# Kernel optimization log

Hardware: AMD Instinct MI355X
Metric: run time of the kernel (lower is better)

The kernel has to match this reference:

```python
import jax, jax.numpy as jnp
import numpy as np

DIM = 384
NUM_HEADS = 8
HEAD_DIM = DIM // NUM_HEADS
SCALE = HEAD_DIM ** -0.5
MLP_HIDDEN = int(DIM * 4.0)
EPS = 1e-6


def setup_inputs() -> dict:
    key = jax.random.key(0)
    ks = jax.random.split(key, 8)
    s = 0.02
    return {
        "x": jax.random.normal(ks[0], (2, DIM, 8, 16, 16), dtype=jnp.float32),
        "g1": jnp.ones((DIM,), jnp.float32),
        "b1": jnp.zeros((DIM,), jnp.float32),
        "Wqkv": jax.random.normal(ks[1], (DIM, 3 * DIM), jnp.float32) * s,  # no bias (qkv_bias=False)
        "Wo": jax.random.normal(ks[2], (DIM, DIM), jnp.float32) * s,
        "bo": jnp.zeros((DIM,), jnp.float32),
        "g2": jnp.ones((DIM,), jnp.float32),
        "b2": jnp.zeros((DIM,), jnp.float32),
        "W1": jax.random.normal(ks[3], (DIM, MLP_HIDDEN), jnp.float32) * s,
        "b1m": jnp.zeros((MLP_HIDDEN,), jnp.float32),
        "W2": jax.random.normal(ks[4], (MLP_HIDDEN, DIM), jnp.float32) * s,
        "b2m": jnp.zeros((DIM,), jnp.float32),
    }


def _layernorm(x, g, b):
    mu = jnp.mean(x, axis=-1, keepdims=True)
    var = jnp.mean(jnp.square(x - mu), axis=-1, keepdims=True)
    return (x - mu) * jax.lax.rsqrt(var + EPS) * g + b


def _attention(h, Wqkv, Wo, bo):
    B, N, C = h.shape
    qkv = h @ Wqkv  # [B, N, 3C]
    qkv = qkv.reshape(B, N, 3, NUM_HEADS, HEAD_DIM).transpose(2, 0, 3, 1, 4)
    q, k, v = qkv[0], qkv[1], qkv[2]  # each [B, H, N, d]
    att = jax.nn.softmax(jnp.einsum('bhxd,bhyd->bhxy', q, k) * SCALE, axis=-1)
    out = jnp.einsum('bhxy,bhyd->bhxd', att, v)  # [B, H, N, d]
    out = out.transpose(0, 2, 1, 3).reshape(B, N, C)
    return out @ Wo + bo


def reference(x, g1, b1, Wqkv, Wo, bo, g2, b2, W1, b1m, W2, b2m):
    B, C, D, H, W = x.shape
    h = x.transpose(0, 2, 3, 4, 1).reshape(B, D * H * W, C)  # b (d h w) c
    h = h + _attention(_layernorm(h, g1, b1), Wqkv, Wo, bo)
    m = _layernorm(h, g2, b2)
    m = jax.nn.gelu(m @ W1 + b1m, approximate=False) @ W2 + b2m
    h = h + m
    return h.reshape(B, D, H, W, C).transpose(0, 4, 1, 2, 3)
```

## Files before the change

kernel.cpp:

```cpp
#include <hip/hip_runtime.h>
#include <hip/hip_bf16.h>
#include <math.h>

#define DIM    384
#define NHEAD  8
#define HDIM   48
#define NTOK   2048
#define BATCH  2
#define TOKS   (BATCH * NTOK)
#define HIDDEN 1536

typedef __bf16 bf16x8 __attribute__((ext_vector_type(8)));
typedef float  f32x4  __attribute__((ext_vector_type(4)));
typedef unsigned short u16;

union bfu { __hip_bfloat16 h; u16 u; };

__device__ __forceinline__ void load_lds16(const void* g, void* l) {
    __builtin_amdgcn_global_load_lds(
        (const __attribute__((address_space(1))) void*)g,
        (__attribute__((address_space(3))) void*)l, 16, 0, 0);
}

__global__ __launch_bounds__(256) void wtrans_all(
    const float* __restrict__ Wqkv, const float* __restrict__ Wo,
    const float* __restrict__ W1,   const float* __restrict__ W2,
    __hip_bfloat16* __restrict__ WqkvT, __hip_bfloat16* __restrict__ WoT,
    __hip_bfloat16* __restrict__ W1T,   __hip_bfloat16* __restrict__ W2T) {
    __shared__ float t[32][33];
    int id = blockIdx.x;
    const float* src; __hip_bfloat16* dst; int R, C;
    if (id < 432)       { src = Wqkv; dst = WqkvT; R = 384;  C = 1152; }
    else if (id < 576)  { id -= 432;  src = Wo;    dst = WoT;  R = 384;  C = 384; }
    else if (id < 1152) { id -= 576;  src = W1;    dst = W1T;  R = 384;  C = 1536; }
    else                { id -= 1152; src = W2;    dst = W2T;  R = 1536; C = 384; }
    int tc = C / 32;
    int i0 = (id / tc) * 32, j0 = (id % tc) * 32;
    int tx = threadIdx.x & 31, ty = threadIdx.x >> 5;
#pragma unroll
    for (int k = 0; k < 32; k += 8)
        t[ty + k][tx] = src[(size_t)(i0 + ty + k) * C + j0 + tx];
    __syncthreads();
#pragma unroll
    for (int k = 0; k < 32; k += 8)
        dst[(size_t)(j0 + ty + k) * R + i0 + tx] = __float2bfloat16(t[tx][ty + k]);
}

__global__ __launch_bounds__(256) void tln(const float* __restrict__ x,
                                           const float* __restrict__ g,
                                           const float* __restrict__ bta,
                                           float* __restrict__ hOut,
                                           __hip_bfloat16* __restrict__ y) {
    __shared__ float t[384 * 33];
    int n0 = blockIdx.x * 32, b = blockIdx.y;
    const float* xb = x + (size_t)b * DIM * NTOK;
    int tid = threadIdx.x;
    for (int idx = tid; idx < 384 * 32; idx += 256) {
        int c = idx >> 5, n = idx & 31;
        t[c * 33 + n] = xb[(size_t)c * NTOK + n0 + n];
    }
    __syncthreads();
    int wid = tid >> 6, lane = tid & 63;
#pragma unroll
    for (int it = 0; it < 8; ++it) {
        int tl = it * 4 + wid;
        float v[6];
        float s = 0.f;
#pragma unroll
        for (int i = 0; i < 6; ++i) { v[i] = t[(lane + 64 * i) * 33 + tl]; s += v[i]; }
#pragma unroll
        for (int o = 32; o; o >>= 1) s += __shfl_xor(s, o, 64);
        float mu = s * (1.f / DIM);
        float s2 = 0.f;
#pragma unroll
        for (int i = 0; i < 6; ++i) { float d = v[i] - mu; s2 += d * d; }
#pragma unroll
        for (int o = 32; o; o >>= 1) s2 += __shfl_xor(s2, o, 64);
        float r = rsqrtf(s2 * (1.f / DIM) + 1e-6f);
        size_t tok = (size_t)b * NTOK + n0 + tl;
#pragma unroll
        for (int i = 0; i < 6; ++i) {
            int c = lane + 64 * i;
            hOut[tok * DIM + c] = v[i];
            y[tok * DIM + c] = __float2bfloat16((v[i] - mu) * r * g[c] + bta[c]);
        }
    }
}

__global__ __launch_bounds__(256) void vtile(const u16* __restrict__ qkv,
                                             unsigned int* __restrict__ vt32) {
    __shared__ u16 t[128 * 49];
    int k0 = blockIdx.x * 128;
    int bh = blockIdx.y;
    int b = bh >> 3, h = bh & 7;
    int tid = threadIdx.x;
    const u16* src = qkv + (size_t)(b * NTOK + k0) * 1152 + 768 + h * 48;
#pragma unroll
    for (int idx = tid; idx < 768; idx += 256) {
        int r = idx / 6, c = idx % 6;
        uint4 v = *(const uint4*)(src + (size_t)r * 1152 + c * 8);
        u16* dst = &t[r * 49 + c * 8];
        dst[0] = (u16)(v.x & 0xffff); dst[1] = (u16)(v.x >> 16);
        dst[2] = (u16)(v.y & 0xffff); dst[3] = (u16)(v.y >> 16);
        dst[4] = (u16)(v.z & 0xffff); dst[5] = (u16)(v.z >> 16);
        dst[6] = (u16)(v.w & 0xffff); dst[7] = (u16)(v.w >> 16);
    }
    __syncthreads();
    unsigned int* outb = vt32 + (((size_t)bh * 48) * 2048 + k0) / 2;
#pragma unroll
    for (int idx = tid; idx < 3072; idx += 256) {
        int d = idx >> 6, pp = idx & 63;
        int k1 = (pp & 3) * 32 + (pp >> 2);
        unsigned int lo = t[k1 * 49 + d];
        unsigned int hi = t[(k1 + 16) * 49 + d];
        outb[(size_t)d * 1024 + pp] = lo | (hi << 16);
    }
}

__global__ __launch_bounds__(256) void ln_kernel(const float* __restrict__ x,
                                                 const float* __restrict__ g,
                                                 const float* __restrict__ bta,
                                                 __hip_bfloat16* __restrict__ y) {
    int wid = threadIdx.x >> 6, lane = threadIdx.x & 63;
    int tok = blockIdx.x * 4 + wid;
    const float* xr = x + (size_t)tok * DIM;
    float v[6];
    float s = 0.f;
#pragma unroll
    for (int i = 0; i < 6; ++i) { v[i] = xr[lane + 64 * i]; s += v[i]; }
#pragma unroll
    for (int o = 32; o; o >>= 1) s += __shfl_xor(s, o, 64);
    float mu = s * (1.f / DIM);
    float s2 = 0.f;
#pragma unroll
    for (int i = 0; i < 6; ++i) { float d = v[i] - mu; s2 += d * d; }
#pragma unroll
    for (int o = 32; o; o >>= 1) s2 += __shfl_xor(s2, o, 64);
    float r = rsqrtf(s2 * (1.f / DIM) + 1e-6f);
    __hip_bfloat16* yr = y + (size_t)tok * DIM;
#pragma unroll
    for (int i = 0; i < 6; ++i) {
        int c = lane + 64 * i;
        yr[c] = __float2bfloat16((v[i] - mu) * r * g[c] + bta[c]);
    }
}

template<bool GELU, bool BF16OUT, bool TRANSOUT>
__global__ __launch_bounds__(256) void gemm_mfma(
    const __hip_bfloat16* __restrict__ A,
    const __hip_bfloat16* __restrict__ BT,
    const float* __restrict__ bias,
    const float* __restrict__ res,
    void* __restrict__ Cout,
    int M, int N, int K) {
    __shared__ __align__(16) u16 As[64 * 32];
    __shared__ __align__(16) u16 Bs[64 * 32];
    int bm = blockIdx.y * 64, bn = blockIdx.x * 64;
    int tid = threadIdx.x;
    int w = tid >> 6, l = tid & 63;
    int m0 = (w >> 1) * 32, n0 = (w & 1) * 32;
    int lm = l & 15, ksel = l >> 4;

    int row = tid >> 2, c16 = tid & 3;
    const __hip_bfloat16* ga = A  + (size_t)(bm + row) * K + c16 * 8;
    const __hip_bfloat16* gb = BT + (size_t)(bn + row) * K + c16 * 8;
    u16* la = &As[tid * 8];
    u16* lb = &Bs[tid * 8];

    f32x4 acc[2][2] = {};
    for (int k0 = 0; k0 < K; k0 += 32) {
        load_lds16(ga + k0, la);
        load_lds16(gb + k0, lb);
        __syncthreads();
        bf16x8 af0 = *(const bf16x8*)&As[(m0 +      lm) * 32 + ksel * 8];
        bf16x8 af1 = *(const bf16x8*)&As[(m0 + 16 + lm) * 32 + ksel * 8];
        bf16x8 bf0 = *(const bf16x8*)&Bs[(n0 +      lm) * 32 + ksel * 8];
        bf16x8 bf1 = *(const bf16x8*)&Bs[(n0 + 16 + lm) * 32 + ksel * 8];
        acc[0][0] = __builtin_amdgcn_mfma_f32_16x16x32_bf16(af0, bf0, acc[0][0], 0, 0, 0);
        acc[0][1] = __builtin_amdgcn_mfma_f32_16x16x32_bf16(af0, bf1, acc[0][1], 0, 0, 0);
        acc[1][0] = __builtin_amdgcn_mfma_f32_16x16x32_bf16(af1, bf0, acc[1][0], 0, 0, 0);
        acc[1][1] = __builtin_amdgcn_mfma_f32_16x16x32_bf16(af1, bf1, acc[1][1], 0, 0, 0);
        __syncthreads();
    }

    if constexpr (TRANSOUT) {
        __shared__ float ct[64 * 65];
#pragma unroll
        for (int i = 0; i < 2; ++i)
#pragma unroll
            for (int j = 0; j < 2; ++j)
#pragma unroll
                for (int r = 0; r < 4; ++r) {
                    int ml = m0 + i * 16 + ksel * 4 + r;
                    int cl = n0 + j * 16 + lm;
                    float v = acc[i][j][r];
                    if (bias) v += bias[bn + cl];
                    if (res)  v += res[(size_t)(bm + ml) * N + bn + cl];
                    ct[ml * 65 + cl] = v;
                }
        __syncthreads();
        int bb = bm >> 11, nb = bm & (NTOK - 1);
        float* outp = (float*)Cout + (size_t)bb * DIM * NTOK + nb;
#pragma unroll
        for (int cl = w; cl < 64; cl += 4)
            outp[(size_t)(bn + cl) * NTOK + l] = ct[l * 65 + cl];
    } else {
#pragma unroll
        for (int i = 0; i < 2; ++i)
#pragma unroll
            for (int j = 0; j < 2; ++j)
#pragma unroll
                for (int r = 0; r < 4; ++r) {
                    int rg = bm + m0 + i * 16 + ksel * 4 + r;
                    int cg = bn + n0 + j * 16 + lm;
                    float v = acc[i][j][r];
                    if (bias) v += bias[cg];
                    if (GELU) v = 0.5f * v * (1.f + erff(v * 0.7071067811865475f));
                    if (res)  v += res[(size_t)rg * N + cg];
                    if (BF16OUT)
                        ((__hip_bfloat16*)Cout)[(size_t)rg * N + cg] = __float2bfloat16(v);
                    else
                        ((float*)Cout)[(size_t)rg * N + cg] = v;
                }
    }
}

#define ATK 128
#define PSTR 136
__global__ __launch_bounds__(256) void attn_mfma(
    const u16* __restrict__ qkv,
    const u16* __restrict__ vt,
    __hip_bfloat16* __restrict__ outp) {
    __shared__ __align__(16) u16 Qs[64 * 72];
    __shared__ __align__(16) u16 Ks[128 * 72];
    __shared__ __align__(16) u16 Vs[48 * PSTR];
    __shared__ __align__(16) u16 Ps[64 * PSTR];
    const int q0 = blockIdx.x * 64;
    const int h = blockIdx.y, b = blockIdx.z;
    const int tid = threadIdx.x;
    const int w = tid >> 6, l = tid & 63, lm = l & 15, quad = l >> 4;

    for (int idx = tid; idx < 128; idx += 256) {
        int r = idx >> 1, c = idx & 1;
        *(uint4*)&Qs[r * 72 + 48 + c * 8] = uint4{0, 0, 0, 0};
    }
    {
        int r = tid >> 1, c = tid & 1;
        *(uint4*)&Ks[r * 72 + 48 + c * 8] = uint4{0, 0, 0, 0};
    }
    const u16* qbase = qkv + (size_t)(b * NTOK + q0) * 1152 + h * 48;
    for (int idx = tid; idx < 384; idx += 256) {
        int r = idx / 6, c = idx % 6;
        *(uint4*)&Qs[r * 72 + c * 8] = *(const uint4*)(qbase + (size_t)r * 1152 + c * 8);
    }
    __syncthreads();

    bf16x8 aq0 = *(const bf16x8*)&Qs[(w * 16 + lm) * 72 +  0 + quad * 8];
    bf16x8 aq1 = *(const bf16x8*)&Qs[(w * 16 + lm) * 72 + 32 + quad * 8];

    float l_i[4] = {0.f, 0.f, 0.f, 0.f};
    f32x4 o_acc[3] = {};

    const u16* kbase = qkv + (size_t)(b * NTOK) * 1152 + 384 + h * 48;
    const u16* vbase = vt + (size_t)(b * NHEAD + h) * 48 * 2048;
    const float sc2 = 0.14433756729740643f * 1.4426950408889634f;

    for (int kt = 0; kt < NTOK / ATK; ++kt) {
        __syncthreads();
#pragma unroll
        for (int idx = tid; idx < 768; idx += 256) {
            int r = idx / 6, c = idx % 6;
            *(uint4*)&Ks[r * 72 + c * 8] =
                *(const uint4*)(kbase + (size_t)(kt * ATK + r) * 1152 + c * 8);
        }
#pragma unroll
        for (int idx = tid; idx < 768; idx += 256) {
            int d = idx >> 4, c = idx & 15;
            *(uint4*)&Vs[d * PSTR + c * 8] =
                *(const uint4*)(vbase + (size_t)d * 2048 + kt * ATK + c * 8);
        }
        __syncthreads();

        f32x4 s[8];
#pragma unroll
        for (int nt = 0; nt < 8; ++nt) {
            bf16x8 kf0 = *(const bf16x8*)&Ks[(nt * 16 + lm) * 72 +  0 + quad * 8];
            bf16x8 kf1 = *(const bf16x8*)&Ks[(nt * 16 + lm) * 72 + 32 + quad * 8];
            f32x4 t = {};
            t = __builtin_amdgcn_mfma_f32_16x16x32_bf16(aq0, kf0, t, 0, 0, 0);
            t = __builtin_amdgcn_mfma_f32_16x16x32_bf16(aq1, kf1, t, 0, 0, 0);
            s[nt] = t;
        }

#pragma unroll
        for (int r = 0; r < 4; ++r) {
            u16 pr[8];
#pragma unroll
            for (int nt = 0; nt < 8; ++nt) {
                float p = exp2f(s[nt][r] * sc2);
                l_i[r] += p;
                bfu cv; cv.h = __float2bfloat16(p);
                pr[nt] = cv.u;
            }
            *(uint4*)&Ps[(w * 16 + quad * 4 + r) * PSTR + lm * 8] = *(const uint4*)pr;
        }

#pragma unroll
        for (int ks = 0; ks < 4; ++ks) {
            bf16x8 pf = *(const bf16x8*)&Ps[(w * 16 + lm) * PSTR + ks * 32 + quad * 8];
#pragma unroll
            for (int nt = 0; nt < 3; ++nt) {
                bf16x8 vf = *(const bf16x8*)&Vs[(nt * 16 + lm) * PSTR + ks * 32 + quad * 8];
                o_acc[nt] = __builtin_amdgcn_mfma_f32_16x16x32_bf16(pf, vf, o_acc[nt], 0, 0, 0);
            }
        }
    }

#pragma unroll
    for (int r = 0; r < 4; ++r) {
        float lsum = l_i[r];
#pragma unroll
        for (int o = 8; o; o >>= 1) lsum += __shfl_xor(lsum, o, 64);
        float inv = 1.f / lsum;
#pragma unroll
        for (int nt = 0; nt < 3; ++nt)
            outp[(size_t)(b * NTOK + q0 + w * 16 + quad * 4 + r) * DIM + h * 48 + nt * 16 + lm]
                = __float2bfloat16(o_acc[nt][r] * inv);
    }
}

extern "C" void kernel_launch(void* const* d_in, const int* in_sizes, int n_in,
                              void* d_out, int out_size, void* d_ws, size_t ws_size,
                              hipStream_t stream) {
    const float* x    = (const float*)d_in[0];
    const float* g1   = (const float*)d_in[1];
    const float* b1   = (const float*)d_in[2];
    const float* Wqkv = (const float*)d_in[3];
    const float* Wo   = (const float*)d_in[4];
    const float* bo   = (const float*)d_in[5];
    const float* g2   = (const float*)d_in[6];
    const float* b2   = (const float*)d_in[7];
    const float* W1   = (const float*)d_in[8];
    const float* b1m  = (const float*)d_in[9];
    const float* W2   = (const float*)d_in[10];
    const float* b2m  = (const float*)d_in[11];
    float* out = (float*)d_out;

    char* p = (char*)d_ws;
    float* bufH = (float*)p;                       p += (size_t)TOKS * DIM * 4;
    char* qkvp = p;
    __hip_bfloat16* bufQKVb = (__hip_bfloat16*)p;  p += (size_t)TOKS * 3 * DIM * 2;
    __hip_bfloat16* bufVT   = (__hip_bfloat16*)p;  p += (size_t)TOKS * DIM * 2;
    __hip_bfloat16* bufNb   = (__hip_bfloat16*)p;  p += (size_t)TOKS * DIM * 2;
    __hip_bfloat16* bufAb   = (__hip_bfloat16*)p;  p += (size_t)TOKS * DIM * 2;
    __hip_bfloat16* WqkvT   = (__hip_bfloat16*)p;  p += (size_t)3 * DIM * DIM * 2;
    __hip_bfloat16* WoT     = (__hip_bfloat16*)p;  p += (size_t)DIM * DIM * 2;
    __hip_bfloat16* W1T     = (__hip_bfloat16*)p;  p += (size_t)HIDDEN * DIM * 2;
    __hip_bfloat16* W2T     = (__hip_bfloat16*)p;  p += (size_t)DIM * HIDDEN * 2;
    __hip_bfloat16* bufHIDb = (__hip_bfloat16*)qkvp;

    wtrans_all<<<1728, 256, 0, stream>>>(Wqkv, Wo, W1, W2, WqkvT, WoT, W1T, W2T);
    tln<<<dim3(NTOK / 32, BATCH), 256, 0, stream>>>(x, g1, b1, bufH, bufNb);
    gemm_mfma<false, true, false><<<dim3(3 * DIM / 64, TOKS / 64), 256, 0, stream>>>(
        bufNb, WqkvT, nullptr, nullptr, bufQKVb, TOKS, 3 * DIM, DIM);
    vtile<<<dim3(NTOK / 128, BATCH * NHEAD), 256, 0, stream>>>(
        (const u16*)bufQKVb, (unsigned int*)bufVT);
    attn_mfma<<<dim3(NTOK / 64, NHEAD, BATCH), 256, 0, stream>>>(
        (const u16*)bufQKVb, (const u16*)bufVT, bufAb);
    gemm_mfma<false, false, false><<<dim3(DIM / 64, TOKS / 64), 256, 0, stream>>>(
        bufAb, WoT, bo, bufH, bufH, TOKS, DIM, DIM);
    ln_kernel<<<TOKS / 4, 256, 0, stream>>>(bufH, g2, b2, bufNb);
    gemm_mfma<true, true, false><<<dim3(HIDDEN / 64, TOKS / 64), 256, 0, stream>>>(
        bufNb, W1T, b1m, nullptr, bufHIDb, TOKS, HIDDEN, DIM);
    gemm_mfma<false, false, true><<<dim3(DIM / 64, TOKS / 64), 256, 0, stream>>>(
        bufHIDb, W2T, b2m, bufH, out, TOKS, DIM, HIDDEN);
}
```

Measured before the change: 223.4 us.

## Split attention key tiles across wave pairs and double GEMM K-step

The attention kernel now launches 512 threads per block, with two waves per 16-query chunk each handling half of every 128-key tile. Their partial outputs and row sums are combined through shared memory at the end. The V-transpose permutation is changed to match the new P layout. Separately, the GEMM loads two 32-wide K slices per barrier pair, which halves the number of synchronisations. The aim is more waves in flight for attention and less barrier overhead in the GEMMs, at the cost of extra LDS use and a final cross-wave reduction.

```diff
diff --git a/kernel.cpp b/kernel.cpp
--- a/kernel.cpp
+++ b/kernel.cpp
@@ -110,7 +110,7 @@
 #pragma unroll
     for (int idx = tid; idx < 3072; idx += 256) {
         int d = idx >> 6, pp = idx & 63;
-        int k1 = (pp & 3) * 32 + (pp >> 2);
+        int k1 = (pp >> 5) * 64 + (pp & 1) * 32 + ((pp >> 1) & 15);
         unsigned int lo = t[k1 * 49 + d];
         unsigned int hi = t[(k1 + 16) * 49 + d];
         outb[(size_t)d * 1024 + pp] = lo | (hi << 16);
@@ -153,8 +153,8 @@
     const float* __restrict__ res,
     void* __restrict__ Cout,
     int M, int N, int K) {
-    __shared__ __align__(16) u16 As[64 * 32];
-    __shared__ __align__(16) u16 Bs[64 * 32];
+    __shared__ __align__(16) u16 As[2][64 * 32];
+    __shared__ __align__(16) u16 Bs[2][64 * 32];
     int bm = blockIdx.y * 64, bn = blockIdx.x * 64;
     int tid = threadIdx.x;
     int w = tid >> 6, l = tid & 63;
@@ -164,22 +164,25 @@
     int row = tid >> 2, c16 = tid & 3;
     const __hip_bfloat16* ga = A  + (size_t)(bm + row) * K + c16 * 8;
     const __hip_bfloat16* gb = BT + (size_t)(bn + row) * K + c16 * 8;
-    u16* la = &As[tid * 8];
-    u16* lb = &Bs[tid * 8];
 
     f32x4 acc[2][2] = {};
-    for (int k0 = 0; k0 < K; k0 += 32) {
-        load_lds16(ga + k0, la);
-        load_lds16(gb + k0, lb);
-        __syncthreads();
-        bf16x8 af0 = *(const bf16x8*)&As[(m0 +      lm) * 32 + ksel * 8];
-        bf16x8 af1 = *(const bf16x8*)&As[(m0 + 16 + lm) * 32 + ksel * 8];
-        bf16x8 bf0 = *(const bf16x8*)&Bs[(n0 +      lm) * 32 + ksel * 8];
-        bf16x8 bf1 = *(const bf16x8*)&Bs[(n0 + 16 + lm) * 32 + ksel * 8];
-        acc[0][0] = __builtin_amdgcn_mfma_f32_16x16x32_bf16(af0, bf0, acc[0][0], 0, 0, 0);
-        acc[0][1] = __builtin_amdgcn_mfma_f32_16x16x32_bf16(af0, bf1, acc[0][1], 0, 0, 0);
-        acc[1][0] = __builtin_amdgcn_mfma_f32_16x16x32_bf16(af1, bf0, acc[1][0], 0, 0, 0);
-        acc[1][1] = __builtin_amdgcn_mfma_f32_16x16x32_bf16(af1, bf1, acc[1][1], 0, 0, 0);
+    for (int k0 = 0; k0 < K; k0 += 64) {
+        load_lds16(ga + k0,      &As[0][tid * 8]);
+        load_lds16(ga + k0 + 32, &As[1][tid * 8]);
+        load_lds16(gb + k0,      &Bs[0][tid * 8]);
+        load_lds16(gb + k0 + 32, &Bs[1][tid * 8]);
+        __syncthreads();
+#pragma unroll
+        for (int kk = 0; kk < 2; ++kk) {
+            bf16x8 af0 = *(const bf16x8*)&As[kk][(m0 +      lm) * 32 + ksel * 8];
+            bf16x8 af1 = *(const bf16x8*)&As[kk][(m0 + 16 + lm) * 32 + ksel * 8];
+            bf16x8 bf0 = *(const bf16x8*)&Bs[kk][(n0 +      lm) * 32 + ksel * 8];
+            bf16x8 bf1 = *(const bf16x8*)&Bs[kk][(n0 + 16 + lm) * 32 + ksel * 8];
+            acc[0][0] = __builtin_amdgcn_mfma_f32_16x16x32_bf16(af0, bf0, acc[0][0], 0, 0, 0);
+            acc[0][1] = __builtin_amdgcn_mfma_f32_16x16x32_bf16(af0, bf1, acc[0][1], 0, 0, 0);
+            acc[1][0] = __builtin_amdgcn_mfma_f32_16x16x32_bf16(af1, bf0, acc[1][0], 0, 0, 0);
+            acc[1][1] = __builtin_amdgcn_mfma_f32_16x16x32_bf16(af1, bf1, acc[1][1], 0, 0, 0);
+        }
         __syncthreads();
     }
 
@@ -227,7 +230,7 @@
 
 #define ATK 128
 #define PSTR 136
-__global__ __launch_bounds__(256) void attn_mfma(
+__global__ __launch_bounds__(512) void attn_mfma(
     const u16* __restrict__ qkv,
     const u16* __restrict__ vt,
     __hip_bfloat16* __restrict__ outp) {
@@ -239,24 +242,25 @@
     const int h = blockIdx.y, b = blockIdx.z;
     const int tid = threadIdx.x;
     const int w = tid >> 6, l = tid & 63, lm = l & 15, quad = l >> 4;
-
-    for (int idx = tid; idx < 128; idx += 256) {
+    const int qc = w >> 1, kh = w & 1;
+
+    for (int idx = tid; idx < 128; idx += 512) {
         int r = idx >> 1, c = idx & 1;
         *(uint4*)&Qs[r * 72 + 48 + c * 8] = uint4{0, 0, 0, 0};
     }
-    {
-        int r = tid >> 1, c = tid & 1;
+    for (int idx = tid; idx < 256; idx += 512) {
+        int r = idx >> 1, c = idx & 1;
         *(uint4*)&Ks[r * 72 + 48 + c * 8] = uint4{0, 0, 0, 0};
     }
     const u16* qbase = qkv + (size_t)(b * NTOK + q0) * 1152 + h * 48;
-    for (int idx = tid; idx < 384; idx += 256) {
+    for (int idx = tid; idx < 384; idx += 512) {
         int r = idx / 6, c = idx % 6;
         *(uint4*)&Qs[r * 72 + c * 8] = *(const uint4*)(qbase + (size_t)r * 1152 + c * 8);
     }
     __syncthreads();
 
-    bf16x8 aq0 = *(const bf16x8*)&Qs[(w * 16 + lm) * 72 +  0 + quad * 8];
-    bf16x8 aq1 = *(const bf16x8*)&Qs[(w * 16 + lm) * 72 + 32 + quad * 8];
+    bf16x8 aq0 = *(const bf16x8*)&Qs[(qc * 16 + lm) * 72 +  0 + quad * 8];
+    bf16x8 aq1 = *(const bf16x8*)&Qs[(qc * 16 + lm) * 72 + 32 + quad * 8];
 
     float l_i[4] = {0.f, 0.f, 0.f, 0.f};
     f32x4 o_acc[3] = {};
@@ -268,46 +272,49 @@
     for (int kt = 0; kt < NTOK / ATK; ++kt) {
         __syncthreads();
 #pragma unroll
-        for (int idx = tid; idx < 768; idx += 256) {
+        for (int idx = tid; idx < 768; idx += 512) {
             int r = idx / 6, c = idx % 6;
             *(uint4*)&Ks[r * 72 + c * 8] =
                 *(const uint4*)(kbase + (size_t)(kt * ATK + r) * 1152 + c * 8);
         }
 #pragma unroll
-        for (int idx = tid; idx < 768; idx += 256) {
+        for (int idx = tid; idx < 768; idx += 512) {
             int d = idx >> 4, c = idx & 15;
             *(uint4*)&Vs[d * PSTR + c * 8] =
                 *(const uint4*)(vbase + (size_t)d * 2048 + kt * ATK + c * 8);
         }
         __syncthreads();
 
-        f32x4 s[8];
-#pragma unroll
-        for (int nt = 0; nt < 8; ++nt) {
+        f32x4 s[4];
+#pragma unroll
+        for (int ntp = 0; ntp < 4; ++ntp) {
+            int nt = kh * 4 + ntp;
             bf16x8 kf0 = *(const bf16x8*)&Ks[(nt * 16 + lm) * 72 +  0 + quad * 8];
             bf16x8 kf1 = *(const bf16x8*)&Ks[(nt * 16 + lm) * 72 + 32 + quad * 8];
             f32x4 t = {};
             t = __builtin_amdgcn_mfma_f32_16x16x32_bf16(aq0, kf0, t, 0, 0, 0);
             t = __builtin_amdgcn_mfma_f32_16x16x32_bf16(aq1, kf1, t, 0, 0, 0);
-            s[nt] = t;
+            s[ntp] = t;
         }
 
 #pragma unroll
         for (int r = 0; r < 4; ++r) {
-            u16 pr[8];
-#pragma unroll
-            for (int nt = 0; nt < 8; ++nt) {
-                float p = exp2f(s[nt][r] * sc2);
+            u16 pr[4];
+#pragma unroll
+            for (int ntp = 0; ntp < 4; ++ntp) {
+                float p = exp2f(s[ntp][r] * sc2);
                 l_i[r] += p;
                 bfu cv; cv.h = __float2bfloat16(p);
-                pr[nt] = cv.u;
+                pr[ntp] = cv.u;
             }
-            *(uint4*)&Ps[(w * 16 + quad * 4 + r) * PSTR + lm * 8] = *(const uint4*)pr;
-        }
-
-#pragma unroll
-        for (int ks = 0; ks < 4; ++ks) {
-            bf16x8 pf = *(const bf16x8*)&Ps[(w * 16 + lm) * PSTR + ks * 32 + quad * 8];
+            *(uint2*)&Ps[(qc * 16 + quad * 4 + r) * PSTR + kh * 64 + lm * 4] =
+                *(const uint2*)pr;
+        }
+
+#pragma unroll
+        for (int ksp = 0; ksp < 2; ++ksp) {
+            int ks = kh * 2 + ksp;
+            bf16x8 pf = *(const bf16x8*)&Ps[(qc * 16 + lm) * PSTR + ks * 32 + quad * 8];
 #pragma unroll
             for (int nt = 0; nt < 3; ++nt) {
                 bf16x8 vf = *(const bf16x8*)&Vs[(nt * 16 + lm) * PSTR + ks * 32 + quad * 8];
@@ -316,16 +323,31 @@
         }
     }
 
-#pragma unroll
-    for (int r = 0; r < 4; ++r) {
-        float lsum = l_i[r];
-#pragma unroll
-        for (int o = 8; o; o >>= 1) lsum += __shfl_xor(lsum, o, 64);
-        float inv = 1.f / lsum;
-#pragma unroll
-        for (int nt = 0; nt < 3; ++nt)
-            outp[(size_t)(b * NTOK + q0 + w * 16 + quad * 4 + r) * DIM + h * 48 + nt * 16 + lm]
-                = __float2bfloat16(o_acc[nt][r] * inv);
+    __syncthreads();
+    float* red = (float*)Ks;
+    if (kh == 1) {
+        f32x4* base = (f32x4*)&red[(qc * 64 + l) * 16];
+        base[0] = o_acc[0]; base[1] = o_acc[1]; base[2] = o_acc[2];
+        f32x4 lv; lv[0] = l_i[0]; lv[1] = l_i[1]; lv[2] = l_i[2]; lv[3] = l_i[3];
+        base[3] = lv;
+    }
+    __syncthreads();
+    if (kh == 0) {
+        f32x4* base = (f32x4*)&red[(qc * 64 + l) * 16];
+        o_acc[0] += base[0]; o_acc[1] += base[1]; o_acc[2] += base[2];
+        f32x4 lv = base[3];
+#pragma unroll
+        for (int r = 0; r < 4; ++r) {
+            float lsum = l_i[r] + lv[r];
+#pragma unroll
+            for (int o = 8; o; o >>= 1) lsum += __shfl_xor(lsum, o, 64);
+            float inv = 1.f / lsum;
+#pragma unroll
+            for (int nt = 0; nt < 3; ++nt)
+                outp[(size_t)(b * NTOK + q0 + qc * 16 + quad * 4 + r) * DIM
+                     + h * 48 + nt * 16 + lm]
+                    = __float2bfloat16(o_acc[nt][r] * inv);
+        }
     }
 }
 
@@ -365,7 +387,7 @@
         bufNb, WqkvT, nullptr, nullptr, bufQKVb, TOKS, 3 * DIM, DIM);
     vtile<<<dim3(NTOK / 128, BATCH * NHEAD), 256, 0, stream>>>(
         (const u16*)bufQKVb, (unsigned int*)bufVT);
-    attn_mfma<<<dim3(NTOK / 64, NHEAD, BATCH), 256, 0, stream>>>(
+    attn_mfma<<<dim3(NTOK / 64, NHEAD, BATCH), 512, 0, stream>>>(
         (const u16*)bufQKVb, (const u16*)bufVT, bufAb);
     gemm_mfma<false, false, false><<<dim3(DIM / 64, TOKS / 64), 256, 0, stream>>>(
         bufAb, WoT, bo, bufH, bufH, TOKS, DIM, DIM);
```

After: 197.8 us. 11.4% less time.
